# Optimization experiments

Hardware: AMD Instinct MI355X
Metric: run time of the kernel (lower is better)

Reference implementation:

```python
import jax, jax.numpy as jnp
import numpy as np

D_MODEL = 1024
N_HEADS = 16
HEAD_DIM = D_MODEL // N_HEADS


def setup_inputs() -> dict:
    key = jax.random.key(0)
    k1, k2, k3 = jax.random.split(key, 3)
    B, S = 4, 2048
    x = jax.random.normal(k1, (B, S, D_MODEL), dtype=jnp.float32)
    # scaled init so logits stay reasonable
    w_qkv = jax.random.normal(k2, (D_MODEL, 3 * D_MODEL), dtype=jnp.float32) / np.sqrt(D_MODEL)
    b_qkv = jnp.zeros((3 * D_MODEL,), dtype=jnp.float32)
    w_out = jax.random.normal(k3, (D_MODEL, D_MODEL), dtype=jnp.float32) / np.sqrt(D_MODEL)
    b_out = jnp.zeros((D_MODEL,), dtype=jnp.float32)
    return {"x": x, "w_qkv": w_qkv, "b_qkv": b_qkv, "w_out": w_out, "b_out": b_out}


def reference(x, w_qkv, b_qkv, w_out, b_out):
    B, S, D = x.shape
    qkv = x @ w_qkv + b_qkv                      # [B,S,3D]
    q, k, v = jnp.split(qkv, 3, axis=-1)
    def split_heads(t):
        return t.reshape(B, S, N_HEADS, HEAD_DIM).transpose(0, 2, 1, 3)  # [B,H,S,d]
    q, k, v = split_heads(q), split_heads(k), split_heads(v)
    a = jnp.einsum('bhsd,bhtd->bhst', q, k)      # [B,H,S,S]
    # causal mask added BEFORE scaling, as in the original module
    causal_mask = jnp.triu(jnp.full((S, S), -jnp.inf, dtype=a.dtype), k=1)
    a = (a + causal_mask) / np.sqrt(HEAD_DIM)
    a = jax.nn.softmax(a, axis=-1)
    z = jnp.einsum('bhst,bhtd->bhsd', a, v)      # [B,H,S,d]
    z = z.transpose(0, 2, 1, 3).reshape(B, S, D)
    return z @ w_out + b_out
```

## Files before the change

### kernel.cpp

```cpp
#include <hip/hip_runtime.h>
#include <hip/hip_bf16.h>
#include <stdint.h>

#define B_   4
#define S_   2048
#define H_   16
#define HD_  64
#define D_   1024

typedef short  short8  __attribute__((ext_vector_type(8)));
typedef float  f32x4   __attribute__((ext_vector_type(4)));
typedef float  f32x16  __attribute__((ext_vector_type(16)));

__device__ __forceinline__ unsigned short f2bf(float f) {
    union { float f; unsigned u; } v; v.f = f;
    unsigned r = v.u + 0x7fffu + ((v.u >> 16) & 1u);
    return (unsigned short)(r >> 16);
}

#if __has_builtin(__builtin_amdgcn_exp2f)
#define EXP2(x) __builtin_amdgcn_exp2f(x)
#else
#define EXP2(x) exp2f(x)
#endif

__device__ __forceinline__ unsigned cvtpk(float lo, float hi) {
    unsigned r;
    asm("v_cvt_pk_bf16_f32 %0, %1, %2" : "=v"(r) : "v"(lo), "v"(hi));
    return r;
}

__device__ __forceinline__ float bq(float v, int srclane) {
    return __int_as_float(__builtin_amdgcn_ds_bpermute(srclane << 2, __float_as_int(v)));
}

__device__ __forceinline__ void pl32swap(unsigned &x, unsigned &y) {
    asm volatile("v_permlane32_swap_b32 %0, %1" : "+v"(x), "+v"(y));
}

#define MFMA32(a, b, c) __builtin_amdgcn_mfma_f32_32x32x16_bf16(a, b, c, 0, 0, 0)

__global__ __launch_bounds__(256) void k_cvt(const float* __restrict__ in,
                                             unsigned short* __restrict__ out) {
    int i = (blockIdx.x * 256 + threadIdx.x) * 4;
    float4 f = *(const float4*)(in + i);
    ushort4 o;
    o.x = f2bf(f.x); o.y = f2bf(f.y); o.z = f2bf(f.z); o.w = f2bf(f.w);
    *(ushort4*)(out + i) = o;
}

__global__ __launch_bounds__(256) void k_transpose_cvt(const float* __restrict__ in,
                                                       unsigned short* __restrict__ out,
                                                       int K, int N) {
    __shared__ float tile[32][33];
    int n0 = blockIdx.x * 32, k0 = blockIdx.y * 32;
    int tx = threadIdx.x, ty = threadIdx.y;
#pragma unroll
    for (int i = 0; i < 32; i += 8)
        tile[ty + i][tx] = in[(size_t)(k0 + ty + i) * N + n0 + tx];
    __syncthreads();
#pragma unroll
    for (int i = 0; i < 32; i += 8)
        out[(size_t)(n0 + ty + i) * K + k0 + tx] = f2bf(tile[tx][ty + i]);
}

__device__ __forceinline__ void async_load16(const unsigned short* g, unsigned short* l) {
    __builtin_amdgcn_global_load_lds(
        (const __attribute__((address_space(1))) unsigned int*)g,
        (__attribute__((address_space(3))) unsigned int*)l, 16, 0, 0);
}

template <int EPI>
__global__ __launch_bounds__(256) void k_gemm(const unsigned short* __restrict__ A,
                                              const unsigned short* __restrict__ BT,
                                              const float* __restrict__ bias,
                                              float* __restrict__ outf,
                                              unsigned short* __restrict__ qb,
                                              unsigned short* __restrict__ kb,
                                              unsigned short* __restrict__ vtb,
                                              int M, int N, int K) {
    __shared__ __attribute__((aligned(16))) unsigned short As0[128 * 64];
    __shared__ __attribute__((aligned(16))) unsigned short Bs0[128 * 64];
    __shared__ __attribute__((aligned(16))) unsigned short As1[128 * 64];
    __shared__ __attribute__((aligned(16))) unsigned short Bs1[128 * 64];
    const int tid = threadIdx.x, wave = tid >> 6, lane = tid & 63;
    const int m0 = blockIdx.y * 128, n0 = blockIdx.x * 128;
    const int wr = wave >> 1, wc = wave & 1;

    int srow[4], scol8[4], sbu[4];
#pragma unroll
    for (int p = 0; p < 4; p++) {
        int bu = p * 256 + wave * 64;
        int u0 = bu + lane;
        sbu[p]   = bu * 8;
        srow[p]  = u0 >> 3;
        scol8[p] = ((u0 & 7) ^ (srow[p] & 7)) * 8;
    }

#define STAGE(AD, BD, KT)                                                           \
    _Pragma("unroll")                                                               \
    for (int p = 0; p < 4; p++) {                                                   \
        async_load16(A  + (size_t)(m0 + srow[p]) * K + (KT) + scol8[p], AD + sbu[p]); \
        async_load16(BT + (size_t)(n0 + srow[p]) * K + (KT) + scol8[p], BD + sbu[p]); \
    }

    f32x4 acc[4][4] = {};

#define COMPUTE(AS, BS)                                                              \
    _Pragma("unroll")                                                                \
    for (int kk = 0; kk < 2; kk++) {                                                 \
        short8 af[4], bf[4];                                                         \
        _Pragma("unroll")                                                            \
        for (int i = 0; i < 4; i++) {                                                \
            int ra = wr * 64 + i * 16 + (lane & 15);                                 \
            int rb = wc * 64 + i * 16 + (lane & 15);                                 \
            int cb = (kk * 32 + (lane >> 4) * 8) * 2;                                \
            af[i] = *(const short8*)((const char*)AS + ra * 128 + (cb ^ ((ra & 7) << 4))); \
            bf[i] = *(const short8*)((const char*)BS + rb * 128 + (cb ^ ((rb & 7) << 4))); \
        }                                                                            \
        __builtin_amdgcn_s_setprio(1);                                               \
        _Pragma("unroll")                                                            \
        for (int i = 0; i < 4; i++)                                                  \
            _Pragma("unroll")                                                        \
            for (int j = 0; j < 4; j++)                                              \
                acc[i][j] = __builtin_amdgcn_mfma_f32_16x16x32_bf16(af[i], bf[j], acc[i][j], 0, 0, 0); \
        __builtin_amdgcn_s_setprio(0);                                               \
    }

    const int NT = K >> 6;
    STAGE(As0, Bs0, 0)
    __syncthreads();
    for (int t = 0; t < NT; t += 2) {
        if (t + 1 < NT) STAGE(As1, Bs1, (t + 1) * 64)
        COMPUTE(As0, Bs0)
        __syncthreads();
        if (t + 2 < NT) STAGE(As0, Bs0, (t + 2) * 64)
        if (t + 1 < NT) {
            COMPUTE(As1, Bs1)
            __syncthreads();
        }
    }
#undef STAGE
#undef COMPUTE

#pragma unroll
    for (int i = 0; i < 4; i++) {
#pragma unroll
        for (int j = 0; j < 4; j++) {
            int n = n0 + wc * 64 + j * 16 + (lane & 15);
            float bv = bias[n];
#pragma unroll
            for (int r = 0; r < 4; r++) {
                int m = m0 + wr * 64 + i * 16 + ((lane >> 4) << 2) + r;
                float val = acc[i][j][r] + bv;
                if (EPI == 0) {
                    int part = n >> 10, rem = n & 1023;
                    int h = rem >> 6, d = rem & 63;
                    int b = m >> 11, s = m & 2047;
                    size_t bh = (size_t)(b * 16 + h);
                    if (part == 2) {
                        size_t off = bh * 131072 +
                            (size_t)(((s >> 5) * 4) + (d >> 5) * 2 + ((s >> 4) & 1)) * 512 +
                            (((d & 31) << 1) + ((s >> 3) & 1)) * 8 + (s & 7);
                        vtb[off] = f2bf(val);
                    } else {
                        size_t off = bh * 131072 +
                            (size_t)(((s >> 5) * 4) + (d >> 4)) * 512 +
                            (((s & 31) << 1) + ((d >> 3) & 1)) * 8 + (d & 7);
                        if (part == 0) qb[off] = f2bf(val * 0.18033688011112042f);
                        else           kb[off] = f2bf(val);
                    }
                } else {
                    outf[(size_t)m * N + n] = val;
                }
            }
        }
    }
}

__device__ __forceinline__ void do_strip(int strip, int bh, int c, int hi,
                                         const unsigned short* __restrict__ QFb,
                                         const unsigned short* __restrict__ KFb,
                                         const unsigned short* __restrict__ VFb,
                                         unsigned short* __restrict__ Z) {
    const int qbase = strip * 32;
    const int b = bh >> 4, h = bh & 15;
    const int lp8 = ((c << 1) + hi) << 3;

    short8 qf[4];
#pragma unroll
    for (int kd = 0; kd < 4; kd++)
        qf[kd] = *(const short8*)(QFb + (strip * 4 + kd) * 512 + lp8);

    f32x16 o0a = {}, o0b = {}, o1a = {}, o1b = {};
    float l_r = 0.f;
    const int nkv = strip + 1;

    short8 kf_cur[4], kf_nxt[4];
#pragma unroll
    for (int kd = 0; kd < 4; kd++)
        kf_cur[kd] = *(const short8*)(KFb + kd * 512 + lp8);

    for (int tt = 0; tt < nkv; ++tt) {
        const int tn = (tt + 1 < nkv) ? (tt + 1) : tt;
#pragma unroll
        for (int kd = 0; kd < 4; kd++)
            kf_nxt[kd] = *(const short8*)(KFb + (tn * 4 + kd) * 512 + lp8);

        short8 vf[2][2];
#pragma unroll
        for (int dt = 0; dt < 2; dt++)
#pragma unroll
            for (int ks = 0; ks < 2; ks++)
                vf[dt][ks] = *(const short8*)(VFb + (tt * 4 + dt * 2 + ks) * 512 + lp8);

        f32x16 sTa = {}, sTb = {};
        sTa = MFMA32(kf_cur[0], qf[0], sTa);
        sTb = MFMA32(kf_cur[2], qf[2], sTb);
        sTa = MFMA32(kf_cur[1], qf[1], sTa);
        sTb = MFMA32(kf_cur[3], qf[3], sTb);
        f32x16 sT;
#pragma unroll
        for (int r = 0; r < 16; r++) sT[r] = sTa[r] + sTb[r];

        if (tt * 32 == qbase) {
#pragma unroll
            for (int r = 0; r < 16; r++) {
                int tl = (r & 3) + 8 * (r >> 2) + 4 * hi;
                if (tl > c) sT[r] = -1e30f;
            }
        }

#pragma unroll
        for (int r = 0; r < 16; r++) sT[r] = EXP2(sT[r]);
        float s0 = sT[0] + sT[8],  s1 = sT[1] + sT[9];
        float s2 = sT[2] + sT[10], s3 = sT[3] + sT[11];
        float s4 = sT[4] + sT[12], s5 = sT[5] + sT[13];
        float s6 = sT[6] + sT[14], s7 = sT[7] + sT[15];
        s0 += s4; s1 += s5; s2 += s6; s3 += s7;
        l_r += (s0 + s2) + (s1 + s3);

        unsigned pk0 = cvtpk(sT[0],  sT[1]);
        unsigned pk1 = cvtpk(sT[2],  sT[3]);
        unsigned pk2 = cvtpk(sT[4],  sT[5]);
        unsigned pk3 = cvtpk(sT[6],  sT[7]);
        unsigned pk4 = cvtpk(sT[8],  sT[9]);
        unsigned pk5 = cvtpk(sT[10], sT[11]);
        unsigned pk6 = cvtpk(sT[12], sT[13]);
        unsigned pk7 = cvtpk(sT[14], sT[15]);
        pl32swap(pk0, pk2);
        pl32swap(pk1, pk3);
        pl32swap(pk4, pk6);
        pl32swap(pk5, pk7);
        union { unsigned u[4]; short8 s; } pa0, pa1;
        pa0.u[0] = pk0; pa0.u[1] = pk1; pa0.u[2] = pk2; pa0.u[3] = pk3;
        pa1.u[0] = pk4; pa1.u[1] = pk5; pa1.u[2] = pk6; pa1.u[3] = pk7;

        o0a = MFMA32(pa0.s, vf[0][0], o0a);
        o1a = MFMA32(pa0.s, vf[1][0], o1a);
        o0b = MFMA32(pa1.s, vf[0][1], o0b);
        o1b = MFMA32(pa1.s, vf[1][1], o1b);

#pragma unroll
        for (int kd = 0; kd < 4; kd++) kf_cur[kd] = kf_nxt[kd];
    }

    l_r += __shfl_xor(l_r, 32);
    float inv = __builtin_amdgcn_rcpf(l_r);
#pragma unroll
    for (int r = 0; r < 16; r++) {
        int crow = (r & 3) + 8 * (r >> 2) + 4 * hi;
        float ib = bq(inv, crow);
        int q = qbase + crow;
        unsigned short* zp = Z + ((size_t)b * S_ + q) * D_ + h * HD_;
        zp[c]      = f2bf((o0a[r] + o0b[r]) * ib);
        zp[32 + c] = f2bf((o1a[r] + o1b[r]) * ib);
    }
}

__global__ __launch_bounds__(64, 2) void k_attn(const unsigned short* __restrict__ QF,
                                                const unsigned short* __restrict__ KF,
                                                const unsigned short* __restrict__ VF,
                                                unsigned short* __restrict__ Z) {
    const int i = blockIdx.x;
    const int bh = (i & 7) * 8 + ((i >> 3) & 7);
    const int pr = i >> 6;
    const int lane = threadIdx.x & 63;
    const int c = lane & 31, hi = lane >> 5;
    const unsigned short* QFb = QF + (size_t)bh * 131072;
    const unsigned short* KFb = KF + (size_t)bh * 131072;
    const unsigned short* VFb = VF + (size_t)bh * 131072;
    do_strip(pr,      bh, c, hi, QFb, KFb, VFb, Z);
    do_strip(63 - pr, bh, c, hi, QFb, KFb, VFb, Z);
}

extern "C" void kernel_launch(void* const* d_in, const int* in_sizes, int n_in,
                              void* d_out, int out_size, void* d_ws, size_t ws_size,
                              hipStream_t stream) {
    const float* x     = (const float*)d_in[0];
    const float* w_qkv = (const float*)d_in[1];
    const float* b_qkv = (const float*)d_in[2];
    const float* w_out = (const float*)d_in[3];
    const float* b_out = (const float*)d_in[4];
    float* out = (float*)d_out;

    char* ws = (char*)d_ws;
    unsigned short* xb    = (unsigned short*)(ws + 0);
    unsigned short* wqkvT = (unsigned short*)(ws + 16777216);
    unsigned short* woutT = (unsigned short*)(ws + 23068672);
    unsigned short* qb    = (unsigned short*)(ws + 25165824);
    unsigned short* kb    = (unsigned short*)(ws + 41943040);
    unsigned short* vtb   = (unsigned short*)(ws + 58720256);
    unsigned short* zb    = xb;

    k_cvt<<<8192, 256, 0, stream>>>(x, xb);
    k_transpose_cvt<<<dim3(96, 32), dim3(32, 8), 0, stream>>>(w_qkv, wqkvT, 1024, 3072);
    k_transpose_cvt<<<dim3(32, 32), dim3(32, 8), 0, stream>>>(w_out, woutT, 1024, 1024);
    k_gemm<0><<<dim3(24, 64), 256, 0, stream>>>(xb, wqkvT, b_qkv, nullptr, qb, kb, vtb,
                                                8192, 3072, 1024);
    k_attn<<<2048, 64, 0, stream>>>(qb, kb, vtb, zb);
    k_gemm<1><<<dim3(8, 64), 256, 0, stream>>>(zb, woutT, b_out, out, nullptr, nullptr, nullptr,
                                               8192, 1024, 1024);
}
```

Baseline: 189.7 us.

## Use 256x256 eight-wave tiles for QKV GEMM with operand swap and vector epilogue

Replaces the QKV projection GEMM with a 512-thread kernel that computes 256x256 tiles, double-buffers LDS with async global-to-LDS loads interleaved with the MFMA phases, and swaps operand roles for the Q/K columns. With the swap, each lane's accumulator holds contiguous head-dim values, so Q/K/V can be written as packed 4-element bf16 stores instead of scalar stores. The larger tile raises data reuse per LDS load and cuts global traffic. In exchange it uses 128KB of LDS and one block per CU, which lowers occupancy and leaves fewer blocks (384) to spread across the CUs.

```diff
diff --git a/kernel.cpp b/kernel.cpp
--- a/kernel.cpp
+++ b/kernel.cpp
@@ -39,6 +39,7 @@
 }
 
 #define MFMA32(a, b, c) __builtin_amdgcn_mfma_f32_32x32x16_bf16(a, b, c, 0, 0, 0)
+#define MFMA16(a, b, c) __builtin_amdgcn_mfma_f32_16x16x32_bf16(a, b, c, 0, 0, 0)
 
 __global__ __launch_bounds__(256) void k_cvt(const float* __restrict__ in,
                                              unsigned short* __restrict__ out) {
@@ -70,15 +71,166 @@
         (__attribute__((address_space(3))) unsigned int*)l, 16, 0, 0);
 }
 
-template <int EPI>
-__global__ __launch_bounds__(256) void k_gemm(const unsigned short* __restrict__ A,
-                                              const unsigned short* __restrict__ BT,
-                                              const float* __restrict__ bias,
-                                              float* __restrict__ outf,
-                                              unsigned short* __restrict__ qb,
-                                              unsigned short* __restrict__ kb,
-                                              unsigned short* __restrict__ vtb,
-                                              int M, int N, int K) {
+__global__ __launch_bounds__(512, 1) void k_gemm8(const unsigned short* __restrict__ A,
+                                                  const unsigned short* __restrict__ BT,
+                                                  const float* __restrict__ bias,
+                                                  unsigned short* __restrict__ qb,
+                                                  unsigned short* __restrict__ kb,
+                                                  unsigned short* __restrict__ vtb,
+                                                  int M, int N, int K) {
+    __shared__ __attribute__((aligned(16))) unsigned short R0s[256 * 64];
+    __shared__ __attribute__((aligned(16))) unsigned short C0s[256 * 64];
+    __shared__ __attribute__((aligned(16))) unsigned short R1s[256 * 64];
+    __shared__ __attribute__((aligned(16))) unsigned short C1s[256 * 64];
+    const int tid = threadIdx.x, wave = tid >> 6, lane = tid & 63;
+    const int wR = wave >> 2, wC = wave & 3;
+    const int m0 = blockIdx.y * 256, n0 = blockIdx.x * 256;
+    const bool tposed = (n0 < 2048);
+
+    const unsigned short* RG = tposed ? (BT + (size_t)n0 * K) : (A + (size_t)m0 * K);
+    const unsigned short* CG = tposed ? (A + (size_t)m0 * K) : (BT + (size_t)n0 * K);
+
+    const int rbase = wave * 8 + (lane >> 3);
+    const int scol8 = ((lane & 7) ^ ((lane >> 3) & 7)) * 8;
+    const int sdst  = wave * 512;
+    const int q15 = lane & 15, q4 = (lane >> 4) << 2;
+    const int cbase0 = ((lane >> 4) * 16) ^ ((lane & 7) << 4);
+    const int cbase1 = (64 + (lane >> 4) * 16) ^ ((lane & 7) << 4);
+
+    f32x4 acc[2][2][4][2] = {};
+
+#pragma unroll
+    for (int p = 0; p < 4; ++p) {
+        const unsigned short* g = (p & 1) ? CG : RG;
+        unsigned short* l = (p & 1) ? C0s : R0s;
+        const int h = p >> 1;
+#pragma unroll
+        for (int L = 0; L < 2; ++L) {
+            int row = h * 128 + L * 64 + rbase;
+            async_load16(g + (size_t)row * K + scol8, l + h * 8192 + L * 4096 + sdst);
+        }
+    }
+    asm volatile("s_waitcnt vmcnt(0)" ::: "memory");
+    __builtin_amdgcn_s_barrier();
+
+    const int NT = K >> 6;
+    for (int t = 0; t < NT; ++t) {
+        const unsigned short* Rb = (t & 1) ? R1s : R0s;
+        const unsigned short* Cb = (t & 1) ? C1s : C0s;
+        unsigned short* Rw = (t & 1) ? R0s : R1s;
+        unsigned short* Cw = (t & 1) ? C0s : C1s;
+        const int more = (t + 1 < NT);
+        const int ktn = (t + 1) * 64;
+#pragma unroll
+        for (int p = 0; p < 4; ++p) {
+            const int mh = p & 1, nh = p >> 1;
+            short8 rf[4][2], cf[2][2];
+#pragma unroll
+            for (int i = 0; i < 4; ++i) {
+                int rr = mh * 128 + wR * 64 + i * 16 + q15;
+                rf[i][0] = *(const short8*)((const char*)Rb + rr * 128 + cbase0);
+                rf[i][1] = *(const short8*)((const char*)Rb + rr * 128 + cbase1);
+            }
+#pragma unroll
+            for (int j = 0; j < 2; ++j) {
+                int cc = nh * 128 + wC * 32 + j * 16 + q15;
+                cf[j][0] = *(const short8*)((const char*)Cb + cc * 128 + cbase0);
+                cf[j][1] = *(const short8*)((const char*)Cb + cc * 128 + cbase1);
+            }
+            if (more) {
+                const unsigned short* g = (p & 1) ? CG : RG;
+                unsigned short* l = (p & 1) ? Cw : Rw;
+                const int h = p >> 1;
+#pragma unroll
+                for (int L = 0; L < 2; ++L) {
+                    int row = h * 128 + L * 64 + rbase;
+                    async_load16(g + (size_t)row * K + ktn + scol8, l + h * 8192 + L * 4096 + sdst);
+                }
+                asm volatile("s_waitcnt vmcnt(4)" ::: "memory");
+            } else {
+                asm volatile("s_waitcnt vmcnt(0)" ::: "memory");
+            }
+            __builtin_amdgcn_s_barrier();
+            asm volatile("s_waitcnt lgkmcnt(0)" ::: "memory");
+            __builtin_amdgcn_sched_barrier(0);
+            __builtin_amdgcn_s_setprio(1);
+#pragma unroll
+            for (int i = 0; i < 4; ++i)
+#pragma unroll
+                for (int j = 0; j < 2; ++j) {
+                    acc[mh][nh][i][j] = MFMA16(rf[i][0], cf[j][0], acc[mh][nh][i][j]);
+                    acc[mh][nh][i][j] = MFMA16(rf[i][1], cf[j][1], acc[mh][nh][i][j]);
+                }
+            __builtin_amdgcn_s_setprio(0);
+            asm volatile("" ::: "memory");
+            __builtin_amdgcn_s_barrier();
+        }
+    }
+
+    if (tposed) {
+        unsigned short* dst = (n0 < 1024) ? qb : kb;
+        const float scale = (n0 < 1024) ? 0.18033688011112042f : 1.0f;
+#pragma unroll
+        for (int mh = 0; mh < 2; ++mh)
+#pragma unroll
+        for (int i = 0; i < 4; ++i) {
+            int nr = n0 + mh * 128 + wR * 64 + i * 16 + q4;
+            float4 bv4 = *(const float4*)(bias + nr);
+            int d0 = nr & 63, h = (nr & 1023) >> 6;
+#pragma unroll
+            for (int nh = 0; nh < 2; ++nh)
+#pragma unroll
+            for (int j = 0; j < 2; ++j) {
+                int mc = m0 + nh * 128 + wC * 32 + j * 16 + q15;
+                int b = mc >> 11, s = mc & 2047;
+                size_t bh = (size_t)(b * 16 + h);
+                f32x4 a = acc[mh][nh][i][j];
+                ushort4 o;
+                o.x = f2bf((a[0] + bv4.x) * scale);
+                o.y = f2bf((a[1] + bv4.y) * scale);
+                o.z = f2bf((a[2] + bv4.z) * scale);
+                o.w = f2bf((a[3] + bv4.w) * scale);
+                size_t off = bh * 131072 +
+                    (size_t)((s >> 5) * 4 + (d0 >> 4)) * 512 +
+                    ((s & 31) * 2 + ((d0 >> 3) & 1)) * 8 + (d0 & 7);
+                *(ushort4*)(dst + off) = o;
+            }
+        }
+    } else {
+#pragma unroll
+        for (int mh = 0; mh < 2; ++mh)
+#pragma unroll
+        for (int i = 0; i < 4; ++i) {
+            int mr = m0 + mh * 128 + wR * 64 + i * 16 + q4;
+            int b = mr >> 11, s0 = mr & 2047;
+#pragma unroll
+            for (int nh = 0; nh < 2; ++nh)
+#pragma unroll
+            for (int j = 0; j < 2; ++j) {
+                int nc = n0 + nh * 128 + wC * 32 + j * 16 + q15;
+                int rem = nc & 1023, h = rem >> 6, d = rem & 63;
+                float bv = bias[nc];
+                f32x4 a = acc[mh][nh][i][j];
+                ushort4 o;
+                o.x = f2bf(a[0] + bv);
+                o.y = f2bf(a[1] + bv);
+                o.z = f2bf(a[2] + bv);
+                o.w = f2bf(a[3] + bv);
+                size_t bh = (size_t)(b * 16 + h);
+                size_t off = bh * 131072 +
+                    (size_t)((s0 >> 5) * 4 + (d >> 5) * 2 + ((s0 >> 4) & 1)) * 512 +
+                    (((d & 31) << 1) + ((s0 >> 3) & 1)) * 8 + (s0 & 7);
+                *(ushort4*)(vtb + off) = o;
+            }
+        }
+    }
+}
+
+__global__ __launch_bounds__(256) void k_gemm_out(const unsigned short* __restrict__ A,
+                                                  const unsigned short* __restrict__ BT,
+                                                  const float* __restrict__ bias,
+                                                  float* __restrict__ outf,
+                                                  int M, int N, int K) {
     __shared__ __attribute__((aligned(16))) unsigned short As0[128 * 64];
     __shared__ __attribute__((aligned(16))) unsigned short Bs0[128 * 64];
     __shared__ __attribute__((aligned(16))) unsigned short As1[128 * 64];
@@ -123,7 +275,7 @@
         for (int i = 0; i < 4; i++)                                                  \
             _Pragma("unroll")                                                        \
             for (int j = 0; j < 4; j++)                                              \
-                acc[i][j] = __builtin_amdgcn_mfma_f32_16x16x32_bf16(af[i], bf[j], acc[i][j], 0, 0, 0); \
+                acc[i][j] = MFMA16(af[i], bf[j], acc[i][j]);                         \
         __builtin_amdgcn_s_setprio(0);                                               \
     }
 
@@ -152,27 +304,7 @@
 #pragma unroll
             for (int r = 0; r < 4; r++) {
                 int m = m0 + wr * 64 + i * 16 + ((lane >> 4) << 2) + r;
-                float val = acc[i][j][r] + bv;
-                if (EPI == 0) {
-                    int part = n >> 10, rem = n & 1023;
-                    int h = rem >> 6, d = rem & 63;
-                    int b = m >> 11, s = m & 2047;
-                    size_t bh = (size_t)(b * 16 + h);
-                    if (part == 2) {
-                        size_t off = bh * 131072 +
-                            (size_t)(((s >> 5) * 4) + (d >> 5) * 2 + ((s >> 4) & 1)) * 512 +
-                            (((d & 31) << 1) + ((s >> 3) & 1)) * 8 + (s & 7);
-                        vtb[off] = f2bf(val);
-                    } else {
-                        size_t off = bh * 131072 +
-                            (size_t)(((s >> 5) * 4) + (d >> 4)) * 512 +
-                            (((s & 31) << 1) + ((d >> 3) & 1)) * 8 + (d & 7);
-                        if (part == 0) qb[off] = f2bf(val * 0.18033688011112042f);
-                        else           kb[off] = f2bf(val);
-                    }
-                } else {
-                    outf[(size_t)m * N + n] = val;
-                }
+                outf[(size_t)m * N + n] = acc[i][j][r] + bv;
             }
         }
     }
@@ -316,9 +448,8 @@
     k_cvt<<<8192, 256, 0, stream>>>(x, xb);
     k_transpose_cvt<<<dim3(96, 32), dim3(32, 8), 0, stream>>>(w_qkv, wqkvT, 1024, 3072);
     k_transpose_cvt<<<dim3(32, 32), dim3(32, 8), 0, stream>>>(w_out, woutT, 1024, 1024);
-    k_gemm<0><<<dim3(24, 64), 256, 0, stream>>>(xb, wqkvT, b_qkv, nullptr, qb, kb, vtb,
-                                                8192, 3072, 1024);
+    k_gemm8<<<dim3(12, 32), 512, 0, stream>>>(xb, wqkvT, b_qkv, qb, kb, vtb,
+                                              8192, 3072, 1024);
     k_attn<<<2048, 64, 0, stream>>>(qb, kb, vtb, zb);
-    k_gemm<1><<<dim3(8, 64), 256, 0, stream>>>(zb, woutT, b_out, out, nullptr, nullptr, nullptr,
-                                               8192, 1024, 1024);
-}
+    k_gemm_out<<<dim3(8, 64), 256, 0, stream>>>(zb, woutT, b_out, out, 8192, 1024, 1024);
+}
```

Result: faster. 179.3 us (-5.5%).

## Replace QKV GEMM with 256x128 8-wave triple-buffered kernel and vectorized epilogue

Applied to the files above, without the earlier changes.

Splits the QKV projection into a new 512-thread GEMM that uses 256x128 tiles, a three-stage async global-to-LDS pipeline with explicit waitcnt and barrier control, and two launches. Q/K use a transposed operand role so each lane writes four contiguous bf16 values, while V keeps the direct role for its transposed layout. The goal is more data reuse per tile, better overlap of loads with MFMA, and fewer scattered scalar stores in the epilogue. The cost is one resident block per CU (large LDS footprint, launch_bounds 512,1) and hand-tuned synchronisation that hardcodes K=1024.

```diff
diff --git a/kernel.cpp b/kernel.cpp
--- a/kernel.cpp
+++ b/kernel.cpp
@@ -39,6 +39,7 @@
 }
 
 #define MFMA32(a, b, c) __builtin_amdgcn_mfma_f32_32x32x16_bf16(a, b, c, 0, 0, 0)
+#define MFMA16(a, b, c) __builtin_amdgcn_mfma_f32_16x16x32_bf16(a, b, c, 0, 0, 0)
 
 __global__ __launch_bounds__(256) void k_cvt(const float* __restrict__ in,
                                              unsigned short* __restrict__ out) {
@@ -70,15 +71,178 @@
         (__attribute__((address_space(3))) unsigned int*)l, 16, 0, 0);
 }
 
-template <int EPI>
-__global__ __launch_bounds__(256) void k_gemm(const unsigned short* __restrict__ A,
-                                              const unsigned short* __restrict__ BT,
-                                              const float* __restrict__ bias,
-                                              float* __restrict__ outf,
-                                              unsigned short* __restrict__ qb,
-                                              unsigned short* __restrict__ kb,
-                                              unsigned short* __restrict__ vtb,
-                                              int M, int N, int K) {
+template <int TPOSED>
+__global__ __launch_bounds__(512, 1) void k_gemm8(const unsigned short* __restrict__ A,
+                                                  const unsigned short* __restrict__ BT,
+                                                  const float* __restrict__ bias,
+                                                  unsigned short* __restrict__ qb,
+                                                  unsigned short* __restrict__ kb,
+                                                  unsigned short* __restrict__ vtb,
+                                                  int M, int N, int K, int nbase) {
+    __shared__ __attribute__((aligned(16))) unsigned short A0s[256 * 64];
+    __shared__ __attribute__((aligned(16))) unsigned short A1s[256 * 64];
+    __shared__ __attribute__((aligned(16))) unsigned short A2s[256 * 64];
+    __shared__ __attribute__((aligned(16))) unsigned short W0s[128 * 64];
+    __shared__ __attribute__((aligned(16))) unsigned short W1s[128 * 64];
+    __shared__ __attribute__((aligned(16))) unsigned short W2s[128 * 64];
+    const int tid = threadIdx.x, wave = tid >> 6, lane = tid & 63;
+    const int wR = wave >> 2, wC = wave & 3;
+    const int m0 = blockIdx.y * 256, n0 = nbase + blockIdx.x * 128;
+
+    const unsigned short* AG = A + (size_t)m0 * K;
+    const unsigned short* WG = BT + (size_t)n0 * K;
+
+    const int rbase = wave * 8 + (lane >> 3);
+    const int scol8 = ((lane & 7) ^ ((lane >> 3) & 7)) * 8;
+    const int sdst  = wave * 512;
+    const int q15 = lane & 15, q4 = (lane >> 4) << 2;
+    const int cb0 = ((lane >> 4) * 16) ^ ((lane & 7) << 4);
+    const int cb1 = (64 + (lane >> 4) * 16) ^ ((lane & 7) << 4);
+
+    f32x4 acc[2][4][2] = {};
+
+#define STAGE3(SA, SW, KT, KH)                                                        \
+    if ((KH) == 0) {                                                                  \
+        async_load16(AG + (size_t)(rbase)       * K + (KT) + scol8, (SA) + 0 * 4096 + sdst); \
+        async_load16(AG + (size_t)(64 + rbase)  * K + (KT) + scol8, (SA) + 1 * 4096 + sdst); \
+        async_load16(WG + (size_t)(rbase)       * K + (KT) + scol8, (SW) + 0 * 4096 + sdst); \
+    } else {                                                                          \
+        async_load16(AG + (size_t)(128 + rbase) * K + (KT) + scol8, (SA) + 2 * 4096 + sdst); \
+        async_load16(AG + (size_t)(192 + rbase) * K + (KT) + scol8, (SA) + 3 * 4096 + sdst); \
+        async_load16(WG + (size_t)(64 + rbase)  * K + (KT) + scol8, (SW) + 1 * 4096 + sdst); \
+    }
+
+#define PHASEBODY(CA, CW, SA, SW, MORE, KT2, KH, CB)                                  \
+    {                                                                                 \
+        short8 xf[2][4], yf[2][2];                                                    \
+        if (TPOSED) {                                                                 \
+            _Pragma("unroll")                                                         \
+            for (int i = 0; i < 4; ++i)                                               \
+                xf[0][i] = *(const short8*)((const char*)(CW) + (wR * 64 + i * 16 + q15) * 128 + (CB)); \
+            _Pragma("unroll")                                                         \
+            for (int h = 0; h < 2; ++h)                                               \
+                _Pragma("unroll")                                                     \
+                for (int j = 0; j < 2; ++j)                                           \
+                    yf[h][j] = *(const short8*)((const char*)(CA) + (h * 128 + wC * 32 + j * 16 + q15) * 128 + (CB)); \
+        } else {                                                                      \
+            _Pragma("unroll")                                                         \
+            for (int h = 0; h < 2; ++h)                                               \
+                _Pragma("unroll")                                                     \
+                for (int i = 0; i < 4; ++i)                                           \
+                    xf[h][i] = *(const short8*)((const char*)(CA) + (h * 128 + wR * 64 + i * 16 + q15) * 128 + (CB)); \
+            _Pragma("unroll")                                                         \
+            for (int j = 0; j < 2; ++j)                                               \
+                yf[0][j] = *(const short8*)((const char*)(CW) + (wC * 32 + j * 16 + q15) * 128 + (CB)); \
+        }                                                                             \
+        if (MORE) {                                                                   \
+            STAGE3(SA, SW, KT2, KH)                                                   \
+            asm volatile("s_waitcnt vmcnt(6)" ::: "memory");                          \
+        } else {                                                                      \
+            asm volatile("s_waitcnt vmcnt(0)" ::: "memory");                          \
+        }                                                                             \
+        __builtin_amdgcn_s_barrier();                                                 \
+        asm volatile("s_waitcnt lgkmcnt(0)" ::: "memory");                            \
+        __builtin_amdgcn_sched_barrier(0);                                            \
+        __builtin_amdgcn_s_setprio(1);                                                \
+        _Pragma("unroll")                                                             \
+        for (int h = 0; h < 2; ++h)                                                   \
+            _Pragma("unroll")                                                         \
+            for (int i = 0; i < 4; ++i)                                               \
+                _Pragma("unroll")                                                     \
+                for (int j = 0; j < 2; ++j)                                           \
+                    acc[h][i][j] = MFMA16(TPOSED ? xf[0][i] : xf[h][i],               \
+                                          TPOSED ? yf[h][j] : yf[0][j],               \
+                                          acc[h][i][j]);                              \
+        __builtin_amdgcn_s_setprio(0);                                                \
+        asm volatile("" ::: "memory");                                                \
+        __builtin_amdgcn_s_barrier();                                                 \
+    }
+
+#define TILEBODY(CA, CW, SA, SW, TC)                                                  \
+    {                                                                                 \
+        const int more_ = ((TC) + 2) < 16;                                            \
+        const int kt2_ = ((TC) + 2) * 64;                                             \
+        PHASEBODY(CA, CW, SA, SW, more_, kt2_, 0, cb0)                                \
+        PHASEBODY(CA, CW, SA, SW, more_, kt2_, 1, cb1)                                \
+    }
+
+    STAGE3(A0s, W0s, 0, 0)
+    STAGE3(A0s, W0s, 0, 1)
+    STAGE3(A1s, W1s, 64, 0)
+    STAGE3(A1s, W1s, 64, 1)
+    asm volatile("s_waitcnt vmcnt(6)" ::: "memory");
+    __builtin_amdgcn_s_barrier();
+
+    for (int t = 0; t < 15; t += 3) {
+        TILEBODY(A0s, W0s, A2s, W2s, t)
+        TILEBODY(A1s, W1s, A0s, W0s, t + 1)
+        TILEBODY(A2s, W2s, A1s, W1s, t + 2)
+    }
+    TILEBODY(A0s, W0s, A2s, W2s, 15)
+#undef STAGE3
+#undef PHASEBODY
+#undef TILEBODY
+
+    if (TPOSED) {
+        unsigned short* dst = (n0 < 1024) ? qb : kb;
+        const float scale = (n0 < 1024) ? 0.18033688011112042f : 1.0f;
+#pragma unroll
+        for (int i = 0; i < 4; ++i) {
+            int nr = n0 + wR * 64 + i * 16 + q4;
+            float4 bv4 = *(const float4*)(bias + nr);
+            int d0 = nr & 63, hh = (nr & 1023) >> 6;
+#pragma unroll
+            for (int h = 0; h < 2; ++h)
+#pragma unroll
+            for (int j = 0; j < 2; ++j) {
+                int mc = m0 + h * 128 + wC * 32 + j * 16 + q15;
+                int b = mc >> 11, s = mc & 2047;
+                size_t bh = (size_t)(b * 16 + hh);
+                f32x4 a = acc[h][i][j];
+                ushort4 o;
+                o.x = f2bf((a[0] + bv4.x) * scale);
+                o.y = f2bf((a[1] + bv4.y) * scale);
+                o.z = f2bf((a[2] + bv4.z) * scale);
+                o.w = f2bf((a[3] + bv4.w) * scale);
+                size_t off = bh * 131072 +
+                    (size_t)((s >> 5) * 4 + (d0 >> 4)) * 512 +
+                    ((s & 31) * 2 + ((d0 >> 3) & 1)) * 8 + (d0 & 7);
+                *(ushort4*)(dst + off) = o;
+            }
+        }
+    } else {
+#pragma unroll
+        for (int h = 0; h < 2; ++h)
+#pragma unroll
+        for (int i = 0; i < 4; ++i) {
+            int mr = m0 + h * 128 + wR * 64 + i * 16 + q4;
+            int b = mr >> 11, s0 = mr & 2047;
+#pragma unroll
+            for (int j = 0; j < 2; ++j) {
+                int nc = n0 + wC * 32 + j * 16 + q15;
+                int rem = nc & 1023, hh = rem >> 6, d = rem & 63;
+                float bv = bias[nc];
+                f32x4 a = acc[h][i][j];
+                ushort4 o;
+                o.x = f2bf(a[0] + bv);
+                o.y = f2bf(a[1] + bv);
+                o.z = f2bf(a[2] + bv);
+                o.w = f2bf(a[3] + bv);
+                size_t bh = (size_t)(b * 16 + hh);
+                size_t off = bh * 131072 +
+                    (size_t)((s0 >> 5) * 4 + (d >> 5) * 2 + ((s0 >> 4) & 1)) * 512 +
+                    (((d & 31) << 1) + ((s0 >> 3) & 1)) * 8 + (s0 & 7);
+                *(ushort4*)(vtb + off) = o;
+            }
+        }
+    }
+}
+
+__global__ __launch_bounds__(256) void k_gemm_out(const unsigned short* __restrict__ A,
+                                                  const unsigned short* __restrict__ BT,
+                                                  const float* __restrict__ bias,
+                                                  float* __restrict__ outf,
+                                                  int M, int N, int K) {
     __shared__ __attribute__((aligned(16))) unsigned short As0[128 * 64];
     __shared__ __attribute__((aligned(16))) unsigned short Bs0[128 * 64];
     __shared__ __attribute__((aligned(16))) unsigned short As1[128 * 64];
@@ -123,7 +287,7 @@
         for (int i = 0; i < 4; i++)                                                  \
             _Pragma("unroll")                                                        \
             for (int j = 0; j < 4; j++)                                              \
-                acc[i][j] = __builtin_amdgcn_mfma_f32_16x16x32_bf16(af[i], bf[j], acc[i][j], 0, 0, 0); \
+                acc[i][j] = MFMA16(af[i], bf[j], acc[i][j]);                         \
         __builtin_amdgcn_s_setprio(0);                                               \
     }
 
@@ -152,27 +316,7 @@
 #pragma unroll
             for (int r = 0; r < 4; r++) {
                 int m = m0 + wr * 64 + i * 16 + ((lane >> 4) << 2) + r;
-                float val = acc[i][j][r] + bv;
-                if (EPI == 0) {
-                    int part = n >> 10, rem = n & 1023;
-                    int h = rem >> 6, d = rem & 63;
-                    int b = m >> 11, s = m & 2047;
-                    size_t bh = (size_t)(b * 16 + h);
-                    if (part == 2) {
-                        size_t off = bh * 131072 +
-                            (size_t)(((s >> 5) * 4) + (d >> 5) * 2 + ((s >> 4) & 1)) * 512 +
-                            (((d & 31) << 1) + ((s >> 3) & 1)) * 8 + (s & 7);
-                        vtb[off] = f2bf(val);
-                    } else {
-                        size_t off = bh * 131072 +
-                            (size_t)(((s >> 5) * 4) + (d >> 4)) * 512 +
-                            (((s & 31) << 1) + ((d >> 3) & 1)) * 8 + (d & 7);
-                        if (part == 0) qb[off] = f2bf(val * 0.18033688011112042f);
-                        else           kb[off] = f2bf(val);
-                    }
-                } else {
-                    outf[(size_t)m * N + n] = val;
-                }
+                outf[(size_t)m * N + n] = acc[i][j][r] + bv;
             }
         }
     }
@@ -316,9 +460,10 @@
     k_cvt<<<8192, 256, 0, stream>>>(x, xb);
     k_transpose_cvt<<<dim3(96, 32), dim3(32, 8), 0, stream>>>(w_qkv, wqkvT, 1024, 3072);
     k_transpose_cvt<<<dim3(32, 32), dim3(32, 8), 0, stream>>>(w_out, woutT, 1024, 1024);
-    k_gemm<0><<<dim3(24, 64), 256, 0, stream>>>(xb, wqkvT, b_qkv, nullptr, qb, kb, vtb,
-                                                8192, 3072, 1024);
+    k_gemm8<1><<<dim3(16, 32), 512, 0, stream>>>(xb, wqkvT, b_qkv, qb, kb, vtb,
+                                                 8192, 3072, 1024, 0);
+    k_gemm8<0><<<dim3(8, 32), 512, 0, stream>>>(xb, wqkvT, b_qkv, qb, kb, vtb,
+                                                8192, 3072, 1024, 2048);
     k_attn<<<2048, 64, 0, stream>>>(qb, kb, vtb, zb);
-    k_gemm<1><<<dim3(8, 64), 256, 0, stream>>>(zb, woutT, b_out, out, nullptr, nullptr, nullptr,
-                                               8192, 1024, 1024);
-}
+    k_gemm_out<<<dim3(8, 64), 256, 0, stream>>>(zb, woutT, b_out, out, 8192, 1024, 1024);
+}
```

Measured after the change: 172.8 us. 8.9% less time.
